# Kernel tuning notes

Measured on AMD Instinct MI355X. Metric: run time of the kernel, lower is better.

Reference implementation:

```python
import jax, jax.numpy as jnp
import numpy as np

N = 50000
E = 800000
IN_F = 128
OUT_F = 128


def setup_inputs() -> dict:
    key = jax.random.key(0)
    k1, k2, k3, k4, k5 = jax.random.split(key, 5)
    x = jax.random.normal(k1, (N, IN_F), dtype=jnp.float32)
    # sparse adjacency as COO edge list: row = dst (aggregating node), col = src
    edge_index = jax.random.randint(k2, (2, E), 0, N, dtype=jnp.int64)
    edge_weight = jax.random.uniform(k3, (E,), dtype=jnp.float32)
    # nn.Linear(in_features, out_features): W is [out, in], b is [out]
    W = jax.random.normal(k4, (OUT_F, IN_F), dtype=jnp.float32) * (1.0 / np.sqrt(IN_F))
    b = jax.random.normal(k5, (OUT_F,), dtype=jnp.float32) * 0.01
    return {"x": x, "edge_index": edge_index, "edge_weight": edge_weight, "W": W, "b": b}


def reference(x, edge_index, edge_weight, W, b):
    # hidden = self.linear(x)  -> [N, out]
    hidden = jnp.einsum("ni,oi->no", x, W) + b
    # out = adj @ hidden (SpMM): out[dst] += w_e * hidden[src]
    dst = edge_index[0]
    src = edge_index[1]
    msgs = edge_weight[:, None] * hidden[src]  # [E, out]
    out = jax.ops.segment_sum(msgs, dst, num_segments=x.shape[0])
    return out
```

## Files before the change

kernel.cpp:

```cpp
#include <hip/hip_runtime.h>
#include <hip/hip_bf16.h>

#define N_NODES 50000
#define N_EDGES 800000
#define FEAT    128
#define N_TILES (N_NODES / 16)
#define GEMM_BLOCKS 784
#define MAXD    32
#define OVF_CAP 16384
#define NODES_PER_GRP 6250
#define CHUNK   2048
#define NCHUNK  ((N_EDGES + CHUNK - 1) / CHUNK)

using short8  = __attribute__((ext_vector_type(8))) short;
using float4v = __attribute__((ext_vector_type(4))) float;


__device__ __forceinline__ unsigned short f2b(float f) {
    __hip_bfloat16 h = __float2bfloat16(f);
    return __builtin_bit_cast(unsigned short, h);
}

__global__ void k_init(const int* __restrict__ ei, int* __restrict__ flag,
                       int* __restrict__ fill) {
    int i = blockIdx.x * blockDim.x + threadIdx.x;
    if (i < N_NODES) fill[i] = 0;
    if (blockIdx.x == 0 && threadIdx.x < 64) {
        unsigned long long m = __ballot(ei[2 * threadIdx.x + 1] != 0);
        if (threadIdx.x == 0) { flag[0] = (m == 0ULL) ? 1 : 0; flag[1] = 0; }
    }
}

__global__ __launch_bounds__(256) void k_fused(const float* __restrict__ x,
                                               const float* __restrict__ W,
                                               const float* __restrict__ bias,
                                               unsigned short* __restrict__ hidden,
                                               const int* __restrict__ ei,
                                               const float* __restrict__ wt,
                                               int* __restrict__ flag,
                                               int* __restrict__ fill,
                                               unsigned int* __restrict__ slots,
                                               int2* __restrict__ ovf) {
    __shared__ __align__(16) unsigned short Wlds[128 * 136];
    const int t = threadIdx.x;

    if (blockIdx.x < GEMM_BLOCKS) {
        for (int j = 0; j < 16; ++j) {
            int idx4 = j * 256 + t;
            float4v wv = *(const float4v*)(W + (size_t)idx4 * 4);
            int r = (idx4 * 4) >> 7;
            int c = (idx4 * 4) & 127;
            unsigned short* p = &Wlds[r * 136 + c];
            p[0] = f2b(wv[0]); p[1] = f2b(wv[1]); p[2] = f2b(wv[2]); p[3] = f2b(wv[3]);
        }
        __syncthreads();

        const int wave = t >> 6;
        const int lane = t & 63;
        int tile = blockIdx.x * 4 + wave;
        if (tile >= N_TILES) tile = N_TILES - 1;
        const int rowBase = tile * 16;
        const int m    = lane & 15;
        const int quad = lane >> 4;

        float4v acc[8];
        for (int i = 0; i < 8; ++i) acc[i] = (float4v){0.f, 0.f, 0.f, 0.f};

        for (int kk = 0; kk < 4; ++kk) {
            const int k0 = kk * 32 + quad * 8;
            const float* ap = x + (size_t)(rowBase + m) * FEAT + k0;
            float4v a0 = *(const float4v*)(ap);
            float4v a1 = *(const float4v*)(ap + 4);
            short8 af;
            for (int j = 0; j < 4; ++j) { af[j] = (short)f2b(a0[j]); af[4 + j] = (short)f2b(a1[j]); }
            for (int nt = 0; nt < 8; ++nt) {
                short8 bf = *(const short8*)&Wlds[(nt * 16 + m) * 136 + k0];
                acc[nt] = __builtin_amdgcn_mfma_f32_16x16x32_bf16(af, bf, acc[nt], 0, 0, 0);
            }
        }

        const int r0 = rowBase + quad * 4;
        for (int nt = 0; nt < 8; ++nt) {
            const int col = nt * 16 + m;
            const float bc = bias[col];
            for (int r = 0; r < 4; ++r) {
                hidden[(size_t)(r0 + r) * FEAT + col] = f2b(acc[nt][r] + bc);
            }
        }
    } else {
        const int bid = blockIdx.x - GEMM_BLOCKS;
        const int grp = bid & 7;
        const int lo  = grp * NODES_PER_GRP;
        const int hi  = lo + NODES_PER_GRP;
        const int sh  = flag[0];
        const int e0  = (bid >> 3) * CHUNK + t;

        int dsts[8];
        #pragma unroll
        for (int i = 0; i < 8; ++i) {
            int e = e0 + i * 256;
            dsts[i] = (e < N_EDGES) ? ei[(size_t)e << sh] : -1;
        }
        #pragma unroll
        for (int i = 0; i < 8; ++i) {
            int e = e0 + i * 256;
            if (e >= N_EDGES) continue;
            int dst = dsts[i];
            if ((unsigned)dst >= N_NODES) dst = 0;
            if (dst < lo || dst >= hi) continue;
            int src = ei[(size_t)(N_EDGES + e) << sh];
            if ((unsigned)src >= N_NODES) src = 0;
            unsigned int rec = ((unsigned int)f2b(wt[e]) << 16) | (unsigned int)src;
            int pos = atomicAdd(&fill[dst], 1);
            if (pos < MAXD) {
                slots[(size_t)dst * MAXD + pos] = rec;
            } else {
                int op = atomicAdd(&flag[1], 1);
                if (op < OVF_CAP) { int2 r; r.x = dst; r.y = (int)rec; ovf[op] = r; }
            }
        }
    }
}

__global__ __launch_bounds__(256) void k_agg(const int* __restrict__ fill,
                                             const unsigned int* __restrict__ slots,
                                             const unsigned int* __restrict__ hid,
                                             const int* __restrict__ flag,
                                             const int2* __restrict__ ovf,
                                             float* __restrict__ out) {
    const int wave = threadIdx.x >> 6;
    const int lane = threadIdx.x & 63;
    const int node = blockIdx.x * 4 + wave;
    const int grp  = lane >> 4;
    const int sub  = lane & 15;

    const int degf = fill[node];
    const int deg  = (degf > MAXD) ? MAXD : degf;
    const unsigned int* sl = slots + (size_t)node * MAXD;

    float acc[8];
    #pragma unroll
    for (int j = 0; j < 8; ++j) acc[j] = 0.f;

    for (int e = 0; e < deg; e += 4) {
        uint4 recs = *(const uint4*)(sl + e);
        unsigned rec = (grp < 2) ? (grp == 0 ? recs.x : recs.y)
                                 : (grp == 2 ? recs.z : recs.w);
        const bool v = (e + grp) < deg;
        const float w = v ? __uint_as_float(rec & 0xffff0000u) : 0.f;
        const unsigned src = v ? (rec & 0xffffu) : 0u;
        uint4 h = *((const uint4*)(hid + (size_t)src * 64) + sub);
        acc[0] = fmaf(w, __uint_as_float((h.x & 0xffffu) << 16), acc[0]);
        acc[1] = fmaf(w, __uint_as_float(h.x & 0xffff0000u),     acc[1]);
        acc[2] = fmaf(w, __uint_as_float((h.y & 0xffffu) << 16), acc[2]);
        acc[3] = fmaf(w, __uint_as_float(h.y & 0xffff0000u),     acc[3]);
        acc[4] = fmaf(w, __uint_as_float((h.z & 0xffffu) << 16), acc[4]);
        acc[5] = fmaf(w, __uint_as_float(h.z & 0xffff0000u),     acc[5]);
        acc[6] = fmaf(w, __uint_as_float((h.w & 0xffffu) << 16), acc[6]);
        acc[7] = fmaf(w, __uint_as_float(h.w & 0xffff0000u),     acc[7]);
    }

    if (degf > MAXD) {
        int n = flag[1]; if (n > OVF_CAP) n = OVF_CAP;
        for (int i = 0; i < n; ++i) {
            int2 r = ovf[i];
            if (r.x != node || (i & 3) != grp) continue;
            unsigned rec = (unsigned)r.y;
            float w = __uint_as_float(rec & 0xffff0000u);
            unsigned src = rec & 0xffffu;
            uint4 h = *((const uint4*)(hid + (size_t)src * 64) + sub);
            acc[0] = fmaf(w, __uint_as_float((h.x & 0xffffu) << 16), acc[0]);
            acc[1] = fmaf(w, __uint_as_float(h.x & 0xffff0000u),     acc[1]);
            acc[2] = fmaf(w, __uint_as_float((h.y & 0xffffu) << 16), acc[2]);
            acc[3] = fmaf(w, __uint_as_float(h.y & 0xffff0000u),     acc[3]);
            acc[4] = fmaf(w, __uint_as_float((h.z & 0xffffu) << 16), acc[4]);
            acc[5] = fmaf(w, __uint_as_float(h.z & 0xffff0000u),     acc[5]);
            acc[6] = fmaf(w, __uint_as_float((h.w & 0xffffu) << 16), acc[6]);
            acc[7] = fmaf(w, __uint_as_float(h.w & 0xffff0000u),     acc[7]);
        }
    }

    #pragma unroll
    for (int j = 0; j < 8; ++j) {
        float a = acc[j];
        a += __shfl_xor(a, 16, 64);
        a += __shfl_xor(a, 32, 64);
        acc[j] = a;
    }

    if (lane < 16) {
        float* o = out + (size_t)node * FEAT + sub * 8;
        *(float4*)(o)     = make_float4(acc[0], acc[1], acc[2], acc[3]);
        *(float4*)(o + 4) = make_float4(acc[4], acc[5], acc[6], acc[7]);
    }
}

extern "C" void kernel_launch(void* const* d_in, const int* in_sizes, int n_in,
                              void* d_out, int out_size, void* d_ws, size_t ws_size,
                              hipStream_t stream) {
    const float* x  = (const float*)d_in[0];
    const int*   ei = (const int*)d_in[1];
    const float* ew = (const float*)d_in[2];
    const float* W  = (const float*)d_in[3];
    const float* b  = (const float*)d_in[4];
    float* out = (float*)d_out;

    int*  flag = (int*)d_ws;
    int*  fill = flag + 16;
    int2* ovf  = (int2*)(fill + 50048);
    unsigned int* slots = (unsigned int*)(ovf + OVF_CAP);
    unsigned short* hidden = (unsigned short*)(slots + (size_t)N_NODES * MAXD);

    k_init <<<(N_NODES + 255) / 256, 256, 0, stream>>>(ei, flag, fill);
    k_fused<<<GEMM_BLOCKS + NCHUNK * 8, 256, 0, stream>>>(x, W, b, hidden, ei, ew,
                                                          flag, fill, slots, ovf);
    k_agg  <<<N_NODES / 4, 256, 0, stream>>>(fill, slots, (const unsigned int*)hidden,
                                             flag, ovf, out);
}
```

Baseline: 172.0 us.

## Replace init kernel with memset, drop W LDS staging, unroll aggregation loop

Removes the k_init kernel: the workspace is zeroed with hipMemsetAsync and each scatter block recomputes the int64/int32 layout flag with its own ballot. The GEMM blocks no longer stage W in LDS and instead read and convert W fragments straight from global memory per MFMA, which drops the shared-memory footprint and the barrier but re-reads W through cache. The aggregation loop now processes two record groups per iteration so two hidden-row gathers are in flight at once. The memset still goes through the runtime, and the extra global W loads plus bf16 conversions add ALU work to the GEMM blocks.

```diff
diff --git a/kernel.cpp b/kernel.cpp
--- a/kernel.cpp
+++ b/kernel.cpp
@@ -21,16 +21,6 @@
     return __builtin_bit_cast(unsigned short, h);
 }
 
-__global__ void k_init(const int* __restrict__ ei, int* __restrict__ flag,
-                       int* __restrict__ fill) {
-    int i = blockIdx.x * blockDim.x + threadIdx.x;
-    if (i < N_NODES) fill[i] = 0;
-    if (blockIdx.x == 0 && threadIdx.x < 64) {
-        unsigned long long m = __ballot(ei[2 * threadIdx.x + 1] != 0);
-        if (threadIdx.x == 0) { flag[0] = (m == 0ULL) ? 1 : 0; flag[1] = 0; }
-    }
-}
-
 __global__ __launch_bounds__(256) void k_fused(const float* __restrict__ x,
                                                const float* __restrict__ W,
                                                const float* __restrict__ bias,
@@ -41,20 +31,9 @@
                                                int* __restrict__ fill,
                                                unsigned int* __restrict__ slots,
                                                int2* __restrict__ ovf) {
-    __shared__ __align__(16) unsigned short Wlds[128 * 136];
     const int t = threadIdx.x;
 
     if (blockIdx.x < GEMM_BLOCKS) {
-        for (int j = 0; j < 16; ++j) {
-            int idx4 = j * 256 + t;
-            float4v wv = *(const float4v*)(W + (size_t)idx4 * 4);
-            int r = (idx4 * 4) >> 7;
-            int c = (idx4 * 4) & 127;
-            unsigned short* p = &Wlds[r * 136 + c];
-            p[0] = f2b(wv[0]); p[1] = f2b(wv[1]); p[2] = f2b(wv[2]); p[3] = f2b(wv[3]);
-        }
-        __syncthreads();
-
         const int wave = t >> 6;
         const int lane = t & 63;
         int tile = blockIdx.x * 4 + wave;
@@ -64,6 +43,7 @@
         const int quad = lane >> 4;
 
         float4v acc[8];
+        #pragma unroll
         for (int i = 0; i < 8; ++i) acc[i] = (float4v){0.f, 0.f, 0.f, 0.f};
 
         for (int kk = 0; kk < 4; ++kk) {
@@ -72,9 +52,17 @@
             float4v a0 = *(const float4v*)(ap);
             float4v a1 = *(const float4v*)(ap + 4);
             short8 af;
+            #pragma unroll
             for (int j = 0; j < 4; ++j) { af[j] = (short)f2b(a0[j]); af[4 + j] = (short)f2b(a1[j]); }
+            const float* wp = W + (size_t)m * FEAT + k0;
+            #pragma unroll
             for (int nt = 0; nt < 8; ++nt) {
-                short8 bf = *(const short8*)&Wlds[(nt * 16 + m) * 136 + k0];
+                const float* q = wp + (size_t)nt * 16 * FEAT;
+                float4v b0 = *(const float4v*)(q);
+                float4v b1 = *(const float4v*)(q + 4);
+                short8 bf;
+                #pragma unroll
+                for (int j = 0; j < 4; ++j) { bf[j] = (short)f2b(b0[j]); bf[4 + j] = (short)f2b(b1[j]); }
                 acc[nt] = __builtin_amdgcn_mfma_f32_16x16x32_bf16(af, bf, acc[nt], 0, 0, 0);
             }
         }
@@ -83,6 +71,7 @@
         for (int nt = 0; nt < 8; ++nt) {
             const int col = nt * 16 + m;
             const float bc = bias[col];
+            #pragma unroll
             for (int r = 0; r < 4; ++r) {
                 hidden[(size_t)(r0 + r) * FEAT + col] = f2b(acc[nt][r] + bc);
             }
@@ -92,7 +81,11 @@
         const int grp = bid & 7;
         const int lo  = grp * NODES_PER_GRP;
         const int hi  = lo + NODES_PER_GRP;
-        const int sh  = flag[0];
+
+        const int lane = t & 63;
+        unsigned long long mball = __ballot(ei[2 * lane + 1] != 0);
+        const int sh = (mball == 0ULL) ? 1 : 0;
+
         const int e0  = (bid >> 3) * CHUNK + t;
 
         int dsts[8];
@@ -136,28 +129,46 @@
 
     const int degf = fill[node];
     const int deg  = (degf > MAXD) ? MAXD : degf;
-    const unsigned int* sl = slots + (size_t)node * MAXD;
+    const uint4* sl4 = (const uint4*)(slots + (size_t)node * MAXD);
 
     float acc[8];
     #pragma unroll
     for (int j = 0; j < 8; ++j) acc[j] = 0.f;
 
-    for (int e = 0; e < deg; e += 4) {
-        uint4 recs = *(const uint4*)(sl + e);
-        unsigned rec = (grp < 2) ? (grp == 0 ? recs.x : recs.y)
-                                 : (grp == 2 ? recs.z : recs.w);
-        const bool v = (e + grp) < deg;
-        const float w = v ? __uint_as_float(rec & 0xffff0000u) : 0.f;
-        const unsigned src = v ? (rec & 0xffffu) : 0u;
-        uint4 h = *((const uint4*)(hid + (size_t)src * 64) + sub);
-        acc[0] = fmaf(w, __uint_as_float((h.x & 0xffffu) << 16), acc[0]);
-        acc[1] = fmaf(w, __uint_as_float(h.x & 0xffff0000u),     acc[1]);
-        acc[2] = fmaf(w, __uint_as_float((h.y & 0xffffu) << 16), acc[2]);
-        acc[3] = fmaf(w, __uint_as_float(h.y & 0xffff0000u),     acc[3]);
-        acc[4] = fmaf(w, __uint_as_float((h.z & 0xffffu) << 16), acc[4]);
-        acc[5] = fmaf(w, __uint_as_float(h.z & 0xffff0000u),     acc[5]);
-        acc[6] = fmaf(w, __uint_as_float((h.w & 0xffffu) << 16), acc[6]);
-        acc[7] = fmaf(w, __uint_as_float(h.w & 0xffff0000u),     acc[7]);
+    const int iters = (deg + 3) >> 2;
+    for (int it = 0; it < iters; it += 2) {
+        uint4 ra = sl4[it];
+        uint4 rb = sl4[it | 1];
+        unsigned reca = (grp < 2) ? (grp == 0 ? ra.x : ra.y)
+                                  : (grp == 2 ? ra.z : ra.w);
+        unsigned recb = (grp < 2) ? (grp == 0 ? rb.x : rb.y)
+                                  : (grp == 2 ? rb.z : rb.w);
+        const int  ea = it * 4 + grp;
+        const int  eb = ea + 4;
+        const bool va = ea < deg;
+        const bool vb = eb < deg;
+        const float wa = va ? __uint_as_float(reca & 0xffff0000u) : 0.f;
+        const float wb = vb ? __uint_as_float(recb & 0xffff0000u) : 0.f;
+        const unsigned sa = va ? (reca & 0xffffu) : 0u;
+        const unsigned sb = vb ? (recb & 0xffffu) : 0u;
+        uint4 ha = *((const uint4*)(hid + (size_t)sa * 64) + sub);
+        uint4 hb = *((const uint4*)(hid + (size_t)sb * 64) + sub);
+        acc[0] = fmaf(wa, __uint_as_float((ha.x & 0xffffu) << 16), acc[0]);
+        acc[1] = fmaf(wa, __uint_as_float(ha.x & 0xffff0000u),     acc[1]);
+        acc[2] = fmaf(wa, __uint_as_float((ha.y & 0xffffu) << 16), acc[2]);
+        acc[3] = fmaf(wa, __uint_as_float(ha.y & 0xffff0000u),     acc[3]);
+        acc[4] = fmaf(wa, __uint_as_float((ha.z & 0xffffu) << 16), acc[4]);
+        acc[5] = fmaf(wa, __uint_as_float(ha.z & 0xffff0000u),     acc[5]);
+        acc[6] = fmaf(wa, __uint_as_float((ha.w & 0xffffu) << 16), acc[6]);
+        acc[7] = fmaf(wa, __uint_as_float(ha.w & 0xffff0000u),     acc[7]);
+        acc[0] = fmaf(wb, __uint_as_float((hb.x & 0xffffu) << 16), acc[0]);
+        acc[1] = fmaf(wb, __uint_as_float(hb.x & 0xffff0000u),     acc[1]);
+        acc[2] = fmaf(wb, __uint_as_float((hb.y & 0xffffu) << 16), acc[2]);
+        acc[3] = fmaf(wb, __uint_as_float(hb.y & 0xffff0000u),     acc[3]);
+        acc[4] = fmaf(wb, __uint_as_float((hb.z & 0xffffu) << 16), acc[4]);
+        acc[5] = fmaf(wb, __uint_as_float(hb.z & 0xffff0000u),     acc[5]);
+        acc[6] = fmaf(wb, __uint_as_float((hb.w & 0xffffu) << 16), acc[6]);
+        acc[7] = fmaf(wb, __uint_as_float(hb.w & 0xffff0000u),     acc[7]);
     }
 
     if (degf > MAXD) {
@@ -211,7 +222,8 @@
     unsigned int* slots = (unsigned int*)(ovf + OVF_CAP);
     unsigned short* hidden = (unsigned short*)(slots + (size_t)N_NODES * MAXD);
 
-    k_init <<<(N_NODES + 255) / 256, 256, 0, stream>>>(ei, flag, fill);
+    hipMemsetAsync(d_ws, 0, 64 + 50048 * sizeof(int), stream);
+
     k_fused<<<GEMM_BLOCKS + NCHUNK * 8, 256, 0, stream>>>(x, W, b, hidden, ei, ew,
                                                           flag, fill, slots, ovf);
     k_agg  <<<N_NODES / 4, 256, 0, stream>>>(fill, slots, (const unsigned int*)hidden,
```

Result: no change. 173.4 us (+0.8%).
